# Kernel tuning notes

Measured on AMD Instinct MI355X. Metric: run time of the kernel, lower is better.

## Reference

```python
import jax, jax.numpy as jnp
import numpy as np

# ConvTemporalGraphical (GRIP) forward, eval mode (Dropout = identity).
# All convs are 1x1, i.e. channel-mixing matmuls.

N, V, C_IN, C_OUT, K = 64, 256, 64, 64, 6


def setup_inputs() -> dict:
    key = jax.random.key(0)
    ks = jax.random.split(key, 11)
    x = jax.random.normal(ks[0], (N, C_OUT, V), dtype=jnp.float32)
    xo = jax.random.normal(ks[1], (N, C_IN, V), dtype=jnp.float32)
    A = jax.random.uniform(ks[2], (N, K, V, V), dtype=jnp.float32)
    s = 0.1
    w1 = jax.random.normal(ks[3], (16, 5), dtype=jnp.float32) * s
    b1 = jax.random.normal(ks[4], (16,), dtype=jnp.float32) * s
    w2 = jax.random.normal(ks[5], (32, 16), dtype=jnp.float32) * s
    b2 = jax.random.normal(ks[6], (32,), dtype=jnp.float32) * s
    w3 = jax.random.normal(ks[7], (64, 32), dtype=jnp.float32) * s
    b3 = jax.random.normal(ks[8], (64,), dtype=jnp.float32) * s
    wo = jax.random.normal(ks[9], (C_OUT, C_IN), dtype=jnp.float32) * s
    bo = jax.random.normal(ks[10], (C_OUT,), dtype=jnp.float32) * s
    return {"x": x, "xo": xo, "A": A, "w1": w1, "b1": b1, "w2": w2,
            "b2": b2, "w3": w3, "b3": b3, "wo": wo, "bo": bo}


def reference(x, xo, A, w1, b1, w2, b2, w3, b3, wo, bo):
    # convo: 1x1 Conv1d over channels -> [N, C_OUT, V]
    xo_c = jnp.einsum('niv,oi->nov', xo, wo) + bo[None, :, None]
    # adjmatder on A[:, :5]: 1x1 Conv2d stack 5->16->32->64 (Dropout is eval identity)
    h = jax.nn.relu(jnp.einsum('nivw,oi->novw', A[:, :5], w1) + b1[None, :, None, None])
    h = jax.nn.relu(jnp.einsum('nivw,oi->novw', h, w2) + b2[None, :, None, None])
    A_out = jax.nn.sigmoid(jnp.einsum('nivw,oi->novw', h, w3) + b3[None, :, None, None])
    # neighbor aggregation + sigmoid gating
    posterior_prob = jax.nn.sigmoid(jnp.einsum('ncv,ncvw->ncw', xo_c, A_out))
    return x * posterior_prob, A_out
```

## Files before the change

### kernel.cpp

```cpp
#include <hip/hip_runtime.h>
#include <hip/hip_bf16.h>

#define NV 256
#define NC 64
#define VW 65536
#define NE1 1048576
#define VB 8

typedef __attribute__((ext_vector_type(8))) short bf16x8;
typedef __attribute__((ext_vector_type(16))) float f32x16;
typedef __attribute__((ext_vector_type(2))) unsigned int uint2v;

union fu32 { float f; unsigned int u; };

static __device__ __forceinline__ short f2bf(float x) {
    union { __hip_bfloat16 b; short s; } u;
    u.b = __float2bfloat16(x);
    return u.s;
}
static __device__ __forceinline__ unsigned int cvt_pk_bf16(float a, float b) {
    unsigned int r;
    asm("v_cvt_pk_bf16_f32 %0, %1, %2" : "=v"(r) : "v"(a), "v"(b));
    return r;
}

__global__ __launch_bounds__(256) void k1_xoc(
    const float* __restrict__ xo, const float* __restrict__ wo,
    const float* __restrict__ bo, float* __restrict__ xoc)
{
    const int idx = blockIdx.x * 256 + threadIdx.x;
    const int v = idx & 255;
    const int c = (idx >> 8) & 63;
    const int n = idx >> 14;
    const float* xon = xo + (size_t)n * 64 * NV;
    const float* wrow = wo + c * 64;
    float s = bo[c];
#pragma unroll
    for (int i = 0; i < 64; ++i)
        s = fmaf(wrow[i], xon[i * NV + v], s);
    xoc[idx] = s;
}

__global__ __launch_bounds__(256) void k2_mfma(
    const float* __restrict__ A,
    const float* __restrict__ w1, const float* __restrict__ b1,
    const float* __restrict__ w2, const float* __restrict__ b2,
    const float* __restrict__ w3, const float* __restrict__ b3,
    const float* __restrict__ xoc,
    float* __restrict__ Aout, float* __restrict__ post)
{
    __shared__ float xocs[NC][VB];

    const int t    = threadIdx.x;
    const int wt   = t >> 6;
    const int lane = t & 63;
    const int lo   = lane & 31;
    const int hi   = lane >> 5;
    const int vbase = blockIdx.x * VB;
    const int n    = blockIdx.y;
    const int w0   = wt << 6;

    for (int e = t; e < NC * VB; e += 256) {
        const int c = e >> 3, j = e & (VB - 1);
        xocs[c][j] = xoc[(size_t)n * (NC * NV) + c * NV + vbase + j];
    }
    __syncthreads();

    bf16x8 af[2][2];
#pragma unroll
    for (int ct = 0; ct < 2; ++ct)
#pragma unroll
        for (int h = 0; h < 2; ++h) {
            const float* wp = w3 + ((ct << 5) + lo) * 32 + (h << 4) + (hi << 3);
            bf16x8 pk;
#pragma unroll
            for (int e = 0; e < 8; ++e) pk[e] = f2bf(wp[e]);
            af[ct][h] = pk;
        }

    float gacc[2][16][2];
#pragma unroll
    for (int ct = 0; ct < 2; ++ct)
#pragma unroll
        for (int r = 0; r < 16; ++r) {
            gacc[ct][r][0] = 0.0f;
            gacc[ct][r][1] = 0.0f;
        }

    const float* An  = A    + (size_t)n * 6 * VW;
    float*       Aon = Aout + (size_t)n * NC * VW;
    const float NLOG2E = -1.4426950408889634f;

    for (int vi = 0; vi < VB; ++vi) {
        const int v = vbase + vi;

        const float* ap = An + (size_t)v * NV + w0 + lane;
        const float a0 = ap[0];
        const float a1 = ap[VW];
        const float a2 = ap[2 * VW];
        const float a3 = ap[3 * VW];
        const float a4 = ap[4 * VW];

        float h1v[16];
#pragma unroll
        for (int j = 0; j < 16; ++j) {
            float s = b1[j];
            s = fmaf(w1[j * 5 + 0], a0, s);
            s = fmaf(w1[j * 5 + 1], a1, s);
            s = fmaf(w1[j * 5 + 2], a2, s);
            s = fmaf(w1[j * 5 + 3], a3, s);
            s = fmaf(w1[j * 5 + 4], a4, s);
            h1v[j] = fmaxf(s, 0.0f);
        }
        unsigned int h2p[16];
#pragma unroll
        for (int m = 0; m < 16; ++m) {
            float sa = b2[2 * m];
            float sb = b2[2 * m + 1];
#pragma unroll
            for (int i = 0; i < 16; ++i) {
                sa = fmaf(w2[(2 * m) * 16 + i],     h1v[i], sa);
                sb = fmaf(w2[(2 * m + 1) * 16 + i], h1v[i], sb);
            }
            h2p[m] = cvt_pk_bf16(fmaxf(sa, 0.0f), fmaxf(sb, 0.0f));
        }

        union { unsigned int u[4]; bf16x8 v8; } bT0[2], bT1[2];
#pragma unroll
        for (int h = 0; h < 2; ++h)
#pragma unroll
            for (int j = 0; j < 4; ++j) {
                uint2v r = __builtin_amdgcn_permlane32_swap(
                    h2p[8 * h + j], h2p[8 * h + 4 + j], false, false);
                bT0[h].u[j] = r.x;
                bT1[h].u[j] = r.y;
            }

        float* rowp = Aon + (size_t)v * NV + w0 + lane;

#pragma unroll
        for (int ct = 0; ct < 2; ++ct) {
            f32x16 d0, d1;
#pragma unroll
            for (int r = 0; r < 16; ++r) { d0[r] = 0.0f; d1[r] = 0.0f; }
            d0 = __builtin_amdgcn_mfma_f32_32x32x16_bf16(af[ct][0], bT0[0].v8, d0, 0, 0, 0);
            d0 = __builtin_amdgcn_mfma_f32_32x32x16_bf16(af[ct][1], bT0[1].v8, d0, 0, 0, 0);
            d1 = __builtin_amdgcn_mfma_f32_32x32x16_bf16(af[ct][0], bT1[0].v8, d1, 0, 0, 0);
            d1 = __builtin_amdgcn_mfma_f32_32x32x16_bf16(af[ct][1], bT1[1].v8, d1, 0, 0, 0);
#pragma unroll
            for (int r = 0; r < 16; ++r) {
                const int cx = (ct << 5) + (r & 3) + ((r >> 2) << 3);
                const int cy = cx + 4;
                fu32 ux, uy, mx, my;
                ux.f = d0[r]; uy.f = d1[r];
                uint2v m = __builtin_amdgcn_permlane32_swap(ux.u, uy.u, false, false);
                mx.u = m.x; my.u = m.y;
                const float vx = __builtin_amdgcn_rcpf(
                    1.0f + __builtin_amdgcn_exp2f(fmaf(mx.f, NLOG2E, b3[cx] * NLOG2E)));
                const float vy = __builtin_amdgcn_rcpf(
                    1.0f + __builtin_amdgcn_exp2f(fmaf(my.f, NLOG2E, b3[cy] * NLOG2E)));
                __builtin_nontemporal_store(vx, rowp + (size_t)cx * VW);
                __builtin_nontemporal_store(vy, rowp + (size_t)cy * VW);
                gacc[ct][r][0] = fmaf(xocs[cx][vi], vx, gacc[ct][r][0]);
                gacc[ct][r][1] = fmaf(xocs[cy][vi], vy, gacc[ct][r][1]);
            }
        }
    }

    float* pn = post + (size_t)n * (NC * NV) + w0 + lane;
#pragma unroll
    for (int ct = 0; ct < 2; ++ct)
#pragma unroll
        for (int r = 0; r < 16; ++r) {
            const int cx = (ct << 5) + (r & 3) + ((r >> 2) << 3);
            atomicAdd(pn + cx * NV,       gacc[ct][r][0]);
            atomicAdd(pn + (cx + 4) * NV, gacc[ct][r][1]);
        }
}

__global__ __launch_bounds__(256) void k3_gate(
    const float* __restrict__ x, const float* __restrict__ post,
    float* __restrict__ out1)
{
    const int idx = blockIdx.x * 256 + threadIdx.x;
    const float p = 1.0f / (1.0f + __expf(-post[idx]));
    out1[idx] = x[idx] * p;
}

extern "C" void kernel_launch(void* const* d_in, const int* in_sizes, int n_in,
                              void* d_out, int out_size, void* d_ws, size_t ws_size,
                              hipStream_t stream)
{
    const float* x  = (const float*)d_in[0];
    const float* xo = (const float*)d_in[1];
    const float* A  = (const float*)d_in[2];
    const float* w1 = (const float*)d_in[3];
    const float* b1 = (const float*)d_in[4];
    const float* w2 = (const float*)d_in[5];
    const float* b2 = (const float*)d_in[6];
    const float* w3 = (const float*)d_in[7];
    const float* b3 = (const float*)d_in[8];
    const float* wo = (const float*)d_in[9];
    const float* bo = (const float*)d_in[10];

    float* out1 = (float*)d_out;
    float* Aout = (float*)d_out + NE1;

    float* xoc  = (float*)d_ws;
    float* post = (float*)d_ws + NE1;

    hipMemsetAsync(post, 0, (size_t)NE1 * sizeof(float), stream);
    k1_xoc<<<NE1 / 256, 256, 0, stream>>>(xo, wo, bo, xoc);
    k2_mfma<<<dim3(NV / VB, 64), 256, 0, stream>>>(A, w1, b1, w2, b2, w3, b3,
                                                   xoc, Aout, post);
    k3_gate<<<NE1 / 256, 256, 0, stream>>>(x, post, out1);
}
```

Baseline: 287.6 us.

## Move second 1x1 conv layer onto MFMA and prefetch next row of A

The 16->32 layer (w2) was previously 512 scalar FMAs per lane per row. It now runs as two bf16 MFMA 32x32x16 ops, with h1 packed to bf16 and lane-swapped into B-fragment layout. The MFMA outputs are reshuffled with permlane32 swaps to form the B operands for the w3 MFMA. A software prefetch also loads the next v row's five A values one iteration ahead to hide load latency. This cuts VALU work but adds bf16 rounding of h1, which lowers precision.

```diff
diff --git a/kernel.cpp b/kernel.cpp
--- a/kernel.cpp
+++ b/kernel.cpp
@@ -12,6 +12,7 @@
 typedef __attribute__((ext_vector_type(2))) unsigned int uint2v;
 
 union fu32 { float f; unsigned int u; };
+union U4 { unsigned int u[4]; bf16x8 v8; };
 
 static __device__ __forceinline__ short f2bf(float x) {
     union { __hip_bfloat16 b; short s; } u;
@@ -77,6 +78,9 @@
             for (int e = 0; e < 8; ++e) pk[e] = f2bf(wp[e]);
             af[ct][h] = pk;
         }
+    bf16x8 af2;
+#pragma unroll
+    for (int e = 0; e < 8; ++e) af2[e] = f2bf(w2[lo * 16 + (hi << 3) + e]);
 
     float gacc[2][16][2];
 #pragma unroll
@@ -91,50 +95,71 @@
     float*       Aon = Aout + (size_t)n * NC * VW;
     const float NLOG2E = -1.4426950408889634f;
 
+    const float* ap0 = An + (size_t)vbase * NV + w0 + lane;
+    float a0 = ap0[0], a1 = ap0[VW], a2 = ap0[2 * VW],
+          a3 = ap0[3 * VW], a4 = ap0[4 * VW];
+
     for (int vi = 0; vi < VB; ++vi) {
         const int v = vbase + vi;
 
-        const float* ap = An + (size_t)v * NV + w0 + lane;
-        const float a0 = ap[0];
-        const float a1 = ap[VW];
-        const float a2 = ap[2 * VW];
-        const float a3 = ap[3 * VW];
-        const float a4 = ap[4 * VW];
-
-        float h1v[16];
-#pragma unroll
-        for (int j = 0; j < 16; ++j) {
-            float s = b1[j];
-            s = fmaf(w1[j * 5 + 0], a0, s);
-            s = fmaf(w1[j * 5 + 1], a1, s);
-            s = fmaf(w1[j * 5 + 2], a2, s);
-            s = fmaf(w1[j * 5 + 3], a3, s);
-            s = fmaf(w1[j * 5 + 4], a4, s);
-            h1v[j] = fmaxf(s, 0.0f);
-        }
-        unsigned int h2p[16];
-#pragma unroll
-        for (int m = 0; m < 16; ++m) {
-            float sa = b2[2 * m];
-            float sb = b2[2 * m + 1];
-#pragma unroll
-            for (int i = 0; i < 16; ++i) {
-                sa = fmaf(w2[(2 * m) * 16 + i],     h1v[i], sa);
-                sb = fmaf(w2[(2 * m + 1) * 16 + i], h1v[i], sb);
-            }
-            h2p[m] = cvt_pk_bf16(fmaxf(sa, 0.0f), fmaxf(sb, 0.0f));
-        }
-
-        union { unsigned int u[4]; bf16x8 v8; } bT0[2], bT1[2];
-#pragma unroll
-        for (int h = 0; h < 2; ++h)
-#pragma unroll
-            for (int j = 0; j < 4; ++j) {
-                uint2v r = __builtin_amdgcn_permlane32_swap(
-                    h2p[8 * h + j], h2p[8 * h + 4 + j], false, false);
-                bT0[h].u[j] = r.x;
-                bT1[h].u[j] = r.y;
-            }
+        const int vn = (vi + 1 < VB) ? (vi + 1) : vi;
+        const float* apn = ap0 + (size_t)vn * NV;
+        const float na0 = apn[0], na1 = apn[VW], na2 = apn[2 * VW],
+                    na3 = apn[3 * VW], na4 = apn[4 * VW];
+
+        unsigned int h1p[8];
+#pragma unroll
+        for (int m = 0; m < 8; ++m) {
+            float sa = b1[2 * m];
+            float sb = b1[2 * m + 1];
+            sa = fmaf(w1[(2 * m) * 5 + 0], a0, sa);
+            sa = fmaf(w1[(2 * m) * 5 + 1], a1, sa);
+            sa = fmaf(w1[(2 * m) * 5 + 2], a2, sa);
+            sa = fmaf(w1[(2 * m) * 5 + 3], a3, sa);
+            sa = fmaf(w1[(2 * m) * 5 + 4], a4, sa);
+            sb = fmaf(w1[(2 * m + 1) * 5 + 0], a0, sb);
+            sb = fmaf(w1[(2 * m + 1) * 5 + 1], a1, sb);
+            sb = fmaf(w1[(2 * m + 1) * 5 + 2], a2, sb);
+            sb = fmaf(w1[(2 * m + 1) * 5 + 3], a3, sb);
+            sb = fmaf(w1[(2 * m + 1) * 5 + 4], a4, sb);
+            h1p[m] = cvt_pk_bf16(fmaxf(sa, 0.0f), fmaxf(sb, 0.0f));
+        }
+
+        U4 b1T0, b1T1;
+#pragma unroll
+        for (int j = 0; j < 4; ++j) {
+            uint2v r = __builtin_amdgcn_permlane32_swap(h1p[j], h1p[4 + j],
+                                                        false, false);
+            b1T0.u[j] = r.x;
+            b1T1.u[j] = r.y;
+        }
+        f32x16 d20, d21;
+#pragma unroll
+        for (int r = 0; r < 16; ++r) {
+            const float bv = b2[(r & 3) + ((r >> 2) << 3) + (hi << 2)];
+            d20[r] = bv; d21[r] = bv;
+        }
+        d20 = __builtin_amdgcn_mfma_f32_32x32x16_bf16(af2, b1T0.v8, d20, 0, 0, 0);
+        d21 = __builtin_amdgcn_mfma_f32_32x32x16_bf16(af2, b1T1.v8, d21, 0, 0, 0);
+
+        unsigned int p[8], q[8];
+#pragma unroll
+        for (int j = 0; j < 8; ++j) {
+            p[j] = cvt_pk_bf16(fmaxf(d20[2 * j], 0.0f), fmaxf(d20[2 * j + 1], 0.0f));
+            q[j] = cvt_pk_bf16(fmaxf(d21[2 * j], 0.0f), fmaxf(d21[2 * j + 1], 0.0f));
+        }
+        U4 b3f[2][2];
+#pragma unroll
+        for (int h = 0; h < 2; ++h) {
+            uint2v r02 = __builtin_amdgcn_permlane32_swap(p[4 * h + 0], p[4 * h + 2], false, false);
+            uint2v r13 = __builtin_amdgcn_permlane32_swap(p[4 * h + 1], p[4 * h + 3], false, false);
+            b3f[0][h].u[0] = r02.x; b3f[0][h].u[2] = r02.y;
+            b3f[0][h].u[1] = r13.x; b3f[0][h].u[3] = r13.y;
+            uint2v s02 = __builtin_amdgcn_permlane32_swap(q[4 * h + 0], q[4 * h + 2], false, false);
+            uint2v s13 = __builtin_amdgcn_permlane32_swap(q[4 * h + 1], q[4 * h + 3], false, false);
+            b3f[1][h].u[0] = s02.x; b3f[1][h].u[2] = s02.y;
+            b3f[1][h].u[1] = s13.x; b3f[1][h].u[3] = s13.y;
+        }
 
         float* rowp = Aon + (size_t)v * NV + w0 + lane;
 
@@ -143,10 +168,10 @@
             f32x16 d0, d1;
 #pragma unroll
             for (int r = 0; r < 16; ++r) { d0[r] = 0.0f; d1[r] = 0.0f; }
-            d0 = __builtin_amdgcn_mfma_f32_32x32x16_bf16(af[ct][0], bT0[0].v8, d0, 0, 0, 0);
-            d0 = __builtin_amdgcn_mfma_f32_32x32x16_bf16(af[ct][1], bT0[1].v8, d0, 0, 0, 0);
-            d1 = __builtin_amdgcn_mfma_f32_32x32x16_bf16(af[ct][0], bT1[0].v8, d1, 0, 0, 0);
-            d1 = __builtin_amdgcn_mfma_f32_32x32x16_bf16(af[ct][1], bT1[1].v8, d1, 0, 0, 0);
+            d0 = __builtin_amdgcn_mfma_f32_32x32x16_bf16(af[ct][0], b3f[0][0].v8, d0, 0, 0, 0);
+            d0 = __builtin_amdgcn_mfma_f32_32x32x16_bf16(af[ct][1], b3f[0][1].v8, d0, 0, 0, 0);
+            d1 = __builtin_amdgcn_mfma_f32_32x32x16_bf16(af[ct][0], b3f[1][0].v8, d1, 0, 0, 0);
+            d1 = __builtin_amdgcn_mfma_f32_32x32x16_bf16(af[ct][1], b3f[1][1].v8, d1, 0, 0, 0);
 #pragma unroll
             for (int r = 0; r < 16; ++r) {
                 const int cx = (ct << 5) + (r & 3) + ((r >> 2) << 3);
@@ -165,6 +190,8 @@
                 gacc[ct][r][1] = fmaf(xocs[cy][vi], vy, gacc[ct][r][1]);
             }
         }
+
+        a0 = na0; a1 = na1; a2 = na2; a3 = na3; a4 = na4;
     }
 
     float* pn = post + (size_t)n * (NC * NV) + w0 + lane;
```

Result: faster. 281.2 us (-2.3%).
